# Kernel optimization log

Measured on AMD Instinct MI355X. Metric: run time of the kernel, lower is better.

## Reference

```python
import jax, jax.numpy as jnp
import numpy as np

H, TD, NUM_NODES = 128, 32, 256
B, N, T = 16, 256, 128


def sinusoidal_pe(t, h, dtype=jnp.float32):
    pos = jnp.arange(t, dtype=dtype)[:, None]                      # [T,1]
    div = jnp.exp(jnp.arange(0, h, 2, dtype=dtype) * (-np.log(10000.0) / h))
    pe = jnp.zeros((t, h), dtype=dtype)
    pe = pe.at[:, 0::2].set(jnp.sin(pos * div))
    pe = pe.at[:, 1::2].set(jnp.cos(pos * div))
    return pe                                                      # [T,H]


def setup_inputs() -> dict:
    key = jax.random.key(0)
    ks = jax.random.split(key, 20)
    lin = lambda k, i, o: jax.random.normal(k, (i, o), jnp.float32) / np.sqrt(i)
    return {
        "xf": jax.random.normal(ks[0], (B, N, T, H), jnp.float32),
        "ex": jax.random.normal(ks[1], (B, T, TD), jnp.float32),
        "nf": jax.random.randint(ks[2], (N,), 0, NUM_NODES),
        "mask": jax.random.randint(ks[3], (B, N, T, H), 0, 2).astype(bool),
        "W_in": lin(ks[4], 3 * H, H), "b_in": jnp.zeros((H,), jnp.float32),
        "W_t": lin(ks[5], TD, H), "b_t": jnp.zeros((H,), jnp.float32),
        "E_node": jax.random.normal(ks[6], (NUM_NODES, H), jnp.float32),
        "W_q": lin(ks[7], H, H), "b_q": jnp.zeros((H,), jnp.float32),
        "W_k": lin(ks[8], H, H), "b_k": jnp.zeros((H,), jnp.float32),
        "W_v": lin(ks[9], H, H), "b_v": jnp.zeros((H,), jnp.float32),
        "W_o": lin(ks[10], H, H), "b_o": jnp.zeros((H,), jnp.float32),
    }


def reference(xf, ex, nf, mask, W_in, b_in, W_t, b_t, E_node,
              W_q, b_q, W_k, b_k, W_v, b_v, W_o, b_o):
    b, n, t, h = xf.shape
    # pos-embed + concat(time, node embeds) + linear + GELU (exact erf, like torch F.gelu)
    pe = sinusoidal_pe(t, h, xf.dtype)                              # [T,H]
    time_e = (ex @ W_t + b_t)[:, None, :, :]                        # [B,1,T,H]
    node_e = E_node[nf][None, :, None, :]                           # [1,N,1,H]
    cat = jnp.concatenate([
        xf + pe,
        jnp.broadcast_to(time_e, (b, n, t, h)),
        jnp.broadcast_to(node_e, (b, n, t, h)),
    ], axis=-1)                                                     # [B,N,T,3H]
    x = jax.nn.gelu(cat @ W_in + b_in, approximate=False)           # [B,N,T,H]
    # attention over T per (B,N)
    q = x @ W_q + b_q
    k = x @ W_k + b_k
    v = x @ W_v + b_v
    scores = jnp.einsum('bnsh,bnth->bnst', q, k) * (1.0 / np.sqrt(h))
    A = jnp.nan_to_num(jax.nn.softmax(scores, axis=-1), nan=0.0)    # [B,N,T,T]
    # masked-confidence reduction (detached A in original)
    t_masking = jnp.all(mask, axis=-1)[:, :, None, :].astype(A.dtype)  # [B,N,1,T]
    conf = 1.0 - jnp.sum(jax.lax.stop_gradient(A) * t_masking, axis=-1)  # [B,N,T]
    rec = jnp.einsum('bnst,bnth->bnsh', A, v)                       # [B,N,T,H]
    rec = rec @ W_o + b_o
    return rec, conf
```

## Files before the change

### kernel.cpp

```cpp
#include <hip/hip_runtime.h>
#include <hip/hip_bf16.h>
#include <stdint.h>


typedef __bf16 bf16;
typedef __bf16 bf16x4 __attribute__((ext_vector_type(4)));
typedef __bf16 bf16x8 __attribute__((ext_vector_type(8)));
typedef float  f32x4  __attribute__((ext_vector_type(4)));

#define MFMA16(a, b, c) __builtin_amdgcn_mfma_f32_16x16x32_bf16((a), (b), (c), 0, 0, 0)

__device__ __forceinline__ int allBytesNonzero(unsigned v) {
    return ((v - 0x01010101u) & ~v & 0x80808080u) == 0u;
}

__device__ __forceinline__ bf16x8 cvt8(const float* p) {
    float4 f0 = *reinterpret_cast<const float4*>(p);
    float4 f1 = *reinterpret_cast<const float4*>(p + 4);
    bf16x8 r;
    r[0] = (bf16)f0.x; r[1] = (bf16)f0.y; r[2] = (bf16)f0.z; r[3] = (bf16)f0.w;
    r[4] = (bf16)f1.x; r[5] = (bf16)f1.y; r[6] = (bf16)f1.z; r[7] = (bf16)f1.w;
    return r;
}

__device__ __forceinline__ float gelu_erf(float v) {
    float x  = v * 0.70710678118654752f;
    float ax = fabsf(x);
    float t  = __builtin_amdgcn_rcpf(1.0f + 0.3275911f * ax);
    float p  = ((((1.061405429f * t - 1.453152027f) * t + 1.421413741f) * t
                 - 0.284496736f) * t + 0.254829592f) * t;
    float er = 1.0f - p * __expf(-ax * ax);
    er = copysignf(er, x);
    return 0.5f * v * (1.0f + er);
}

__global__ void prep_weights(const float* __restrict__ W_in, bf16* __restrict__ dst)
{
    int idx = blockIdx.x * 256 + threadIdx.x;
    int h = idx >> 7, k = idx & 127;
    dst[h * 128 + k] = (bf16)W_in[k * 128 + h];
}

__global__ void prep_G(const float* __restrict__ Wq, const float* __restrict__ Wk,
                       const float* __restrict__ bq, bf16* __restrict__ mstore,
                       float* __restrict__ vvec)
{
    const int a = blockIdx.x, bb = threadIdx.x;
    __shared__ float wqa[128];
    wqa[bb] = Wq[a * 128 + bb];
    __syncthreads();
    float acc = 0.f;
    for (int k = 0; k < 128; ++k) acc += wqa[k] * Wk[bb * 128 + k];
    mstore[a * 128 + bb] = (bf16)acc;
    if (a == 0) {
        float av = 0.f;
        for (int j = 0; j < 128; ++j) av += Wk[bb * 128 + j] * bq[j];
        vvec[bb] = av;
    }
}

__global__ void prep_N(const float* __restrict__ Wv, const float* __restrict__ Wo,
                       const float* __restrict__ bv, const float* __restrict__ bo,
                       bf16* __restrict__ nstore, float* __restrict__ bias2)
{
    const int h = blockIdx.x, h2 = threadIdx.x;
    __shared__ float wvh[128];
    wvh[h2] = Wv[h * 128 + h2];
    __syncthreads();
    float acc = 0.f;
    for (int j = 0; j < 128; ++j) acc += wvh[j] * Wo[j * 128 + h2];
    nstore[h2 * 128 + h] = (bf16)acc;
    if (h == 0) {
        float b2 = 0.f;
        for (int j = 0; j < 128; ++j) b2 += bv[j] * Wo[j * 128 + h2];
        bias2[h2] = b2 + bo[h2];
    }
}

__global__ void prep_npart(const int* __restrict__ nf, const float* __restrict__ E_node,
                           const float* __restrict__ W_in, float* __restrict__ npart)
{
    int n = blockIdx.x, h = threadIdx.x;
    int node = nf[n];
    const float* e = E_node + node * 128;
    float acc = 0.f;
    for (int k = 0; k < 128; ++k) acc += e[k] * W_in[(256 + k) * 128 + h];
    npart[n * 128 + h] = acc;
}

__global__ void prep_bias(const float* __restrict__ ex, const float* __restrict__ W_t,
                          const float* __restrict__ b_t, const float* __restrict__ W_in,
                          const float* __restrict__ b_in, float* __restrict__ biasT)
{
    const int bt = blockIdx.x;
    const int t = bt & 127;
    const int h = threadIdx.x;
    __shared__ float te[128];
    float v = b_t[h];
    const float* exr = ex + (size_t)bt * 32;
    for (int d = 0; d < 32; ++d) v += exr[d] * W_t[d * 128 + h];
    te[h] = v;
    __syncthreads();
    float acc = b_in[h];
    const float ninv = -9.210340371976184f / 128.0f;
    for (int j = 0; j < 64; ++j) {
        float div = expf((float)(2 * j) * ninv);
        float ang = (float)t * div;
        acc += sinf(ang) * W_in[(2 * j) * 128 + h] + cosf(ang) * W_in[(2 * j + 1) * 128 + h];
    }
    for (int k = 0; k < 128; ++k) acc += te[k] * W_in[(128 + k) * 128 + h];
    biasT[(size_t)bt * 128 + h] = acc;
}

#define STAGE_ISSUE(SRC)                                                        \
    {                                                                           \
        _Pragma("unroll")                                                       \
        for (int i = 0; i < 4; ++i)                                             \
            stg[i] = *reinterpret_cast<const bf16x8*>((SRC) + (tid + i * 512) * 8); \
    }
#define STAGE_WRITE()                                                           \
    {                                                                           \
        _Pragma("unroll")                                                       \
        for (int i = 0; i < 4; ++i) {                                           \
            int m_ = tid + i * 512;                                             \
            int row_ = m_ >> 4, slot_ = m_ & 15;                                \
            *reinterpret_cast<bf16x8*>(&sW[row_ * 128 + 8 * (slot_ ^ (row_ & 15))]) = stg[i]; \
        }                                                                       \
    }

__global__ __launch_bounds__(512, 4) void fused_main(
    const float* __restrict__ xf, const unsigned char* __restrict__ mask,
    const bf16* __restrict__ wsW, const float* __restrict__ biasT,
    const float* __restrict__ npart, const float* __restrict__ vvec,
    const float* __restrict__ bias2, float* __restrict__ out)
{
    const bf16* W1T = wsW;
    const bf16* Mst = wsW + 16384;
    const bf16* Nst = wsW + 32768;

    __shared__ bf16 sW[16384];
    __shared__ bf16 sKV[128][136];
    __shared__ bf16 sT[8][16][40];
    __shared__ __align__(16) float sTm[128];
    __shared__ __align__(16) float sWt[128];

    const int bn = blockIdx.x;
    const int b  = bn >> 8;
    const int n  = bn & 255;
    const int tid  = (int)threadIdx.x;
    const int w    = tid >> 6;
    const int lane = tid & 63;
    const int c = lane & 15;
    const int g = lane >> 4;
    const int s0 = w << 4;

    const f32x4 FZ = {0.f, 0.f, 0.f, 0.f};
    bf16x8 stg[4];
    bf16* patch = &sT[w][0][0];

    if (tid < 128) {
        const uint4* mp = reinterpret_cast<const uint4*>(mask + ((size_t)bn * 128 + tid) * 128);
        int ok = 1;
        #pragma unroll
        for (int i = 0; i < 8; ++i) {
            uint4 u = mp[i];
            ok &= allBytesNonzero(u.x) & allBytesNonzero(u.y)
                & allBytesNonzero(u.z) & allBytesNonzero(u.w);
        }
        sTm[tid] = ok ? 1.0f : 0.0f;
    }

    STAGE_ISSUE(W1T);
    bf16x8 af[4];
    {
        const float* xfb = xf + (size_t)bn * 16384;
        #pragma unroll
        for (int kk = 0; kk < 4; ++kk)
            af[kk] = cvt8(xfb + (s0 + c) * 128 + kk * 32 + g * 8);
    }
    STAGE_WRITE();
    __syncthreads();

    STAGE_ISSUE(Mst);
    bf16x8 xb[4];
    {
        f32x4 acc[8];
        #pragma unroll
        for (int ht = 0; ht < 8; ++ht) acc[ht] = FZ;
        #pragma unroll
        for (int kk = 0; kk < 4; ++kk) {
            const int k0 = kk * 32 + g * 8;
            #pragma unroll
            for (int ht = 0; ht < 8; ++ht) {
                bf16x8 aw = *reinterpret_cast<const bf16x8*>(
                    &sW[(ht * 16 + c) * 128 + (k0 ^ ((c & 15) << 3))]);
                acc[ht] = MFMA16(aw, af[kk], acc[ht]);
            }
        }
        const float* biasB = biasT + (size_t)b * 16384;
        const float* npRow = npart + n * 128;
        const int t = s0 + c;
        bf16x4 pk[8];
        #pragma unroll
        for (int ht = 0; ht < 8; ++ht) {
            const int hb = ht * 16 + g * 4;
            const float4 bb  = *reinterpret_cast<const float4*>(biasB + t * 128 + hb);
            const float4 np4 = *reinterpret_cast<const float4*>(npRow + hb);
            const float bbr[4] = {bb.x + np4.x, bb.y + np4.y, bb.z + np4.z, bb.w + np4.w};
            #pragma unroll
            for (int r = 0; r < 4; ++r)
                pk[ht][r] = (bf16)gelu_erf(acc[ht][r] + bbr[r]);
        }
        #pragma unroll
        for (int kk = 0; kk < 4; ++kk) {
            *reinterpret_cast<bf16x4*>(patch + c * 40 + g * 4)      = pk[2 * kk];
            *reinterpret_cast<bf16x4*>(patch + c * 40 + 16 + g * 4) = pk[2 * kk + 1];
            xb[kk] = *reinterpret_cast<const bf16x8*>(patch + c * 40 + g * 8);
        }
    }
    __syncthreads();

    STAGE_WRITE();
    __syncthreads();

    STAGE_ISSUE(Nst);
    {
        f32x4 acc[8];
        #pragma unroll
        for (int ht = 0; ht < 8; ++ht) acc[ht] = FZ;
        #pragma unroll
        for (int kk = 0; kk < 4; ++kk) {
            const int k0 = kk * 32 + g * 8;
            #pragma unroll
            for (int ht = 0; ht < 8; ++ht) {
                bf16x8 aw = *reinterpret_cast<const bf16x8*>(
                    &sW[(ht * 16 + c) * 128 + (k0 ^ ((c & 15) << 3))]);
                acc[ht] = MFMA16(aw, xb[kk], acc[ht]);
            }
        }
        const int t = s0 + c;
        #pragma unroll
        for (int ht = 0; ht < 8; ++ht) {
            bf16x4 pk;
            #pragma unroll
            for (int r = 0; r < 4; ++r) pk[r] = (bf16)acc[ht][r];
            *reinterpret_cast<bf16x4*>(&sKV[t][ht * 16 + g * 4]) = pk;
        }
        float wd = 0.f;
        #pragma unroll
        for (int kk = 0; kk < 4; ++kk) {
            const float4 vA = *reinterpret_cast<const float4*>(vvec + kk * 32 + g * 8);
            const float4 vB = *reinterpret_cast<const float4*>(vvec + kk * 32 + g * 8 + 4);
            wd += (float)xb[kk][0] * vA.x + (float)xb[kk][1] * vA.y
                + (float)xb[kk][2] * vA.z + (float)xb[kk][3] * vA.w
                + (float)xb[kk][4] * vB.x + (float)xb[kk][5] * vB.y
                + (float)xb[kk][6] * vB.z + (float)xb[kk][7] * vB.w;
        }
        wd += __shfl_xor(wd, 16);
        wd += __shfl_xor(wd, 32);
        if (g == 0) sWt[t] = wd;
    }
    __syncthreads();

    STAGE_WRITE();
    __syncthreads();

    const float rs = 0.08838834764831845f;
    float l0 = 1.f;
    bf16x8 xp[4];

    {
        f32x4 sc[8];
        #pragma unroll
        for (int rt = 0; rt < 8; ++rt) sc[rt] = FZ;
        #pragma unroll
        for (int kk = 0; kk < 4; ++kk) {
            const int k0 = kk * 32 + g * 8;
            #pragma unroll
            for (int rt = 0; rt < 8; ++rt) {
                bf16x8 ay = *reinterpret_cast<const bf16x8*>(&sKV[rt * 16 + c][k0]);
                sc[rt] = MFMA16(ay, xb[kk], sc[rt]);
            }
        }
        #pragma unroll
        for (int rt = 0; rt < 8; ++rt) {
            const float4 wt4 = *reinterpret_cast<const float4*>(&sWt[rt * 16 + g * 4]);
            sc[rt][0] += wt4.x; sc[rt][1] += wt4.y;
            sc[rt][2] += wt4.z; sc[rt][3] += wt4.w;
        }
        float m = -3.0e38f;
        #pragma unroll
        for (int rt = 0; rt < 8; ++rt)
            #pragma unroll
            for (int r = 0; r < 4; ++r) m = fmaxf(m, sc[rt][r]);
        m = fmaxf(m, __shfl_xor(m, 16));
        m = fmaxf(m, __shfl_xor(m, 32));
        float ls = 0.f, wsum = 0.f;
        #pragma unroll
        for (int rt = 0; rt < 8; ++rt) {
            const float4 tm4 = *reinterpret_cast<const float4*>(&sTm[rt * 16 + g * 4]);
            const float tmr[4] = {tm4.x, tm4.y, tm4.z, tm4.w};
            #pragma unroll
            for (int r = 0; r < 4; ++r) {
                float p = __expf((sc[rt][r] - m) * rs);
                sc[rt][r] = p;
                ls += p;
                wsum += p * tmr[r];
            }
        }
        ls   += __shfl_xor(ls, 16);   ls   += __shfl_xor(ls, 32);
        wsum += __shfl_xor(wsum, 16); wsum += __shfl_xor(wsum, 32);
        l0 = ls;
        if (g == 0)
            out[(size_t)67108864 + (size_t)bn * 128 + s0 + c] = 1.0f - wsum / ls;
        bf16x4 pkP[8];
        #pragma unroll
        for (int rt = 0; rt < 8; ++rt)
            #pragma unroll
            for (int r = 0; r < 4; ++r) pkP[rt][r] = (bf16)sc[rt][r];
        #pragma unroll
        for (int kk = 0; kk < 4; ++kk) {
            *reinterpret_cast<bf16x4*>(patch + c * 40 + g * 4)      = pkP[2 * kk];
            *reinterpret_cast<bf16x4*>(patch + c * 40 + 16 + g * 4) = pkP[2 * kk + 1];
            xp[kk] = *reinterpret_cast<const bf16x8*>(patch + c * 40 + g * 8);
        }
    }

    bf16x4 vpk[8];
    {
        f32x4 acc[8];
        #pragma unroll
        for (int ct = 0; ct < 8; ++ct) acc[ct] = FZ;
        #pragma unroll
        for (int kk = 0; kk < 4; ++kk) {
            const int k0 = kk * 32 + g * 8;
            #pragma unroll
            for (int ct = 0; ct < 8; ++ct) {
                bf16x8 bw = *reinterpret_cast<const bf16x8*>(
                    &sW[(ct * 16 + c) * 128 + (k0 ^ ((c & 15) << 3))]);
                acc[ct] = MFMA16(xb[kk], bw, acc[ct]);
            }
        }
        #pragma unroll
        for (int ct = 0; ct < 8; ++ct)
            #pragma unroll
            for (int r = 0; r < 4; ++r)
                vpk[ct][r] = (bf16)acc[ct][r];
    }
    __syncthreads();

    {
        #pragma unroll
        for (int ct = 0; ct < 8; ++ct)
            *reinterpret_cast<bf16x4*>(&sKV[ct * 16 + c][s0 + g * 4]) = vpk[ct];
    }
    __syncthreads();

    {
        f32x4 rc[8];
        #pragma unroll
        for (int rt = 0; rt < 8; ++rt) rc[rt] = FZ;
        #pragma unroll
        for (int kk = 0; kk < 4; ++kk) {
            const int k0 = kk * 32 + g * 8;
            #pragma unroll
            for (int rt = 0; rt < 8; ++rt) {
                bf16x8 avf = *reinterpret_cast<const bf16x8*>(&sKV[rt * 16 + c][k0]);
                rc[rt] = MFMA16(avf, xp[kk], rc[rt]);
            }
        }
        const float inv0 = __builtin_amdgcn_rcpf(l0);
        float* outb = out + (size_t)bn * 16384 + (size_t)(s0 + c) * 128;
        #pragma unroll
        for (int rt = 0; rt < 8; ++rt) {
            const int hb = rt * 16 + g * 4;
            const float4 b2 = *reinterpret_cast<const float4*>(bias2 + hb);
            float4 v;
            v.x = rc[rt][0] * inv0 + b2.x;
            v.y = rc[rt][1] * inv0 + b2.y;
            v.z = rc[rt][2] * inv0 + b2.z;
            v.w = rc[rt][3] * inv0 + b2.w;
            *reinterpret_cast<float4*>(outb + hb) = v;
        }
    }
}

extern "C" void kernel_launch(void* const* d_in, const int* in_sizes, int n_in,
                              void* d_out, int out_size, void* d_ws, size_t ws_size,
                              hipStream_t stream)
{
    (void)in_sizes; (void)n_in; (void)out_size; (void)ws_size;
    const float* xf     = (const float*)d_in[0];
    const float* ex     = (const float*)d_in[1];
    const int*   nf     = (const int*)d_in[2];
    const unsigned char* mask = (const unsigned char*)d_in[3];
    const float* W_in   = (const float*)d_in[4];
    const float* b_in   = (const float*)d_in[5];
    const float* W_t    = (const float*)d_in[6];
    const float* b_t    = (const float*)d_in[7];
    const float* E_node = (const float*)d_in[8];
    const float* W_q    = (const float*)d_in[9];
    const float* b_q    = (const float*)d_in[10];
    const float* W_k    = (const float*)d_in[11];
    const float* b_k    = (const float*)d_in[12];
    const float* W_v    = (const float*)d_in[13];
    const float* b_v    = (const float*)d_in[14];
    const float* W_o    = (const float*)d_in[15];
    const float* b_o    = (const float*)d_in[16];
    (void)b_k;
    float* out = (float*)d_out;

    bf16*  wsW    = (bf16*)d_ws;
    bf16*  mstore = wsW + 16384;
    bf16*  nstore = wsW + 32768;
    float* biasT  = (float*)((char*)d_ws + 98304);
    float* npart  = (float*)((char*)d_ws + 1146880);
    float* vvec   = (float*)((char*)d_ws + 1277952);
    float* bias2  = (float*)((char*)d_ws + 1278464);

    prep_weights<<<64, 256, 0, stream>>>(W_in, wsW);
    prep_G<<<128, 128, 0, stream>>>(W_q, W_k, b_q, mstore, vvec);
    prep_N<<<128, 128, 0, stream>>>(W_v, W_o, b_v, b_o, nstore, bias2);
    prep_npart<<<256, 128, 0, stream>>>(nf, E_node, W_in, npart);
    prep_bias<<<2048, 128, 0, stream>>>(ex, W_t, b_t, W_in, b_in, biasT);
    fused_main<<<4096, 512, 0, stream>>>(xf, mask, wsW, biasT, npart,
                                         vvec, bias2, out);
}
```

Before: 255.0 us.

## Merge prep kernels, precompute PE sin/cos, raise MFMA priority, move V projection earlier

Four small weight-prep kernels become one launch that picks its job from the block index, which cuts launch overhead. prep_bias now computes the sinusoidal sin/cos values once per block into shared memory instead of once per thread. In the main kernel, MFMA loops are wrapped in s_setprio to favour matrix issue, and the V projection runs before the softmax so it can overlap the exp work. The softmax exponent also becomes a single fma. These changes raise register pressure in the fused section because vpk is held live longer.

```diff
diff --git a/kernel.cpp b/kernel.cpp
--- a/kernel.cpp
+++ b/kernel.cpp
@@ -34,58 +34,52 @@
     return 0.5f * v * (1.0f + er);
 }
 
-__global__ void prep_weights(const float* __restrict__ W_in, bf16* __restrict__ dst)
+__global__ void prep_all(const float* __restrict__ W_in, const float* __restrict__ Wq,
+                         const float* __restrict__ Wk, const float* __restrict__ bq,
+                         const float* __restrict__ Wv, const float* __restrict__ Wo,
+                         const float* __restrict__ bv, const float* __restrict__ bo,
+                         const int* __restrict__ nf, const float* __restrict__ E_node,
+                         bf16* __restrict__ wsW, bf16* __restrict__ mstore,
+                         bf16* __restrict__ nstore, float* __restrict__ vvec,
+                         float* __restrict__ bias2, float* __restrict__ npart)
 {
-    int idx = blockIdx.x * 256 + threadIdx.x;
-    int h = idx >> 7, k = idx & 127;
-    dst[h * 128 + k] = (bf16)W_in[k * 128 + h];
-}
-
-__global__ void prep_G(const float* __restrict__ Wq, const float* __restrict__ Wk,
-                       const float* __restrict__ bq, bf16* __restrict__ mstore,
-                       float* __restrict__ vvec)
-{
-    const int a = blockIdx.x, bb = threadIdx.x;
-    __shared__ float wqa[128];
-    wqa[bb] = Wq[a * 128 + bb];
-    __syncthreads();
-    float acc = 0.f;
-    for (int k = 0; k < 128; ++k) acc += wqa[k] * Wk[bb * 128 + k];
-    mstore[a * 128 + bb] = (bf16)acc;
-    if (a == 0) {
-        float av = 0.f;
-        for (int j = 0; j < 128; ++j) av += Wk[bb * 128 + j] * bq[j];
-        vvec[bb] = av;
-    }
-}
-
-__global__ void prep_N(const float* __restrict__ Wv, const float* __restrict__ Wo,
-                       const float* __restrict__ bv, const float* __restrict__ bo,
-                       bf16* __restrict__ nstore, float* __restrict__ bias2)
-{
-    const int h = blockIdx.x, h2 = threadIdx.x;
-    __shared__ float wvh[128];
-    wvh[h2] = Wv[h * 128 + h2];
-    __syncthreads();
-    float acc = 0.f;
-    for (int j = 0; j < 128; ++j) acc += wvh[j] * Wo[j * 128 + h2];
-    nstore[h2 * 128 + h] = (bf16)acc;
-    if (h == 0) {
-        float b2 = 0.f;
-        for (int j = 0; j < 128; ++j) b2 += bv[j] * Wo[j * 128 + h2];
-        bias2[h2] = b2 + bo[h2];
-    }
-}
-
-__global__ void prep_npart(const int* __restrict__ nf, const float* __restrict__ E_node,
-                           const float* __restrict__ W_in, float* __restrict__ npart)
-{
-    int n = blockIdx.x, h = threadIdx.x;
-    int node = nf[n];
-    const float* e = E_node + node * 128;
-    float acc = 0.f;
-    for (int k = 0; k < 128; ++k) acc += e[k] * W_in[(256 + k) * 128 + h];
-    npart[n * 128 + h] = acc;
+    const int blk = blockIdx.x, t = threadIdx.x;
+    if (blk < 128) {
+        wsW[blk * 128 + t] = (bf16)W_in[t * 128 + blk];
+    } else if (blk < 256) {
+        const int a = blk - 128;
+        __shared__ float wqa[128];
+        wqa[t] = Wq[a * 128 + t];
+        __syncthreads();
+        float acc = 0.f;
+        for (int k = 0; k < 128; ++k) acc += wqa[k] * Wk[t * 128 + k];
+        mstore[a * 128 + t] = (bf16)acc;
+        if (a == 0) {
+            float av = 0.f;
+            for (int j = 0; j < 128; ++j) av += Wk[t * 128 + j] * bq[j];
+            vvec[t] = av;
+        }
+    } else if (blk < 384) {
+        const int h = blk - 256;
+        __shared__ float wvh[128];
+        wvh[t] = Wv[h * 128 + t];
+        __syncthreads();
+        float acc = 0.f;
+        for (int j = 0; j < 128; ++j) acc += wvh[j] * Wo[j * 128 + t];
+        nstore[t * 128 + h] = (bf16)acc;
+        if (h == 0) {
+            float b2 = 0.f;
+            for (int j = 0; j < 128; ++j) b2 += bv[j] * Wo[j * 128 + t];
+            bias2[t] = b2 + bo[t];
+        }
+    } else {
+        const int n = blk - 384;
+        int node = nf[n];
+        const float* e = E_node + node * 128;
+        float acc = 0.f;
+        for (int k = 0; k < 128; ++k) acc += e[k] * W_in[(256 + k) * 128 + t];
+        npart[n * 128 + t] = acc;
+    }
 }
 
 __global__ void prep_bias(const float* __restrict__ ex, const float* __restrict__ W_t,
@@ -96,18 +90,22 @@
     const int t = bt & 127;
     const int h = threadIdx.x;
     __shared__ float te[128];
+    __shared__ float sn[64], cs[64];
     float v = b_t[h];
     const float* exr = ex + (size_t)bt * 32;
     for (int d = 0; d < 32; ++d) v += exr[d] * W_t[d * 128 + h];
     te[h] = v;
+    if (h < 64) {
+        const float ninv = -9.210340371976184f / 128.0f;
+        float div = expf((float)(2 * h) * ninv);
+        float ang = (float)t * div;
+        sn[h] = sinf(ang);
+        cs[h] = cosf(ang);
+    }
     __syncthreads();
     float acc = b_in[h];
-    const float ninv = -9.210340371976184f / 128.0f;
-    for (int j = 0; j < 64; ++j) {
-        float div = expf((float)(2 * j) * ninv);
-        float ang = (float)t * div;
-        acc += sinf(ang) * W_in[(2 * j) * 128 + h] + cosf(ang) * W_in[(2 * j + 1) * 128 + h];
-    }
+    for (int j = 0; j < 64; ++j)
+        acc += sn[j] * W_in[(2 * j) * 128 + h] + cs[j] * W_in[(2 * j + 1) * 128 + h];
     for (int k = 0; k < 128; ++k) acc += te[k] * W_in[(128 + k) * 128 + h];
     biasT[(size_t)bt * 128 + h] = acc;
 }
@@ -187,6 +185,7 @@
         f32x4 acc[8];
         #pragma unroll
         for (int ht = 0; ht < 8; ++ht) acc[ht] = FZ;
+        __builtin_amdgcn_s_setprio(1);
         #pragma unroll
         for (int kk = 0; kk < 4; ++kk) {
             const int k0 = kk * 32 + g * 8;
@@ -197,6 +196,7 @@
                 acc[ht] = MFMA16(aw, af[kk], acc[ht]);
             }
         }
+        __builtin_amdgcn_s_setprio(0);
         const float* biasB = biasT + (size_t)b * 16384;
         const float* npRow = npart + n * 128;
         const int t = s0 + c;
@@ -228,6 +228,7 @@
         f32x4 acc[8];
         #pragma unroll
         for (int ht = 0; ht < 8; ++ht) acc[ht] = FZ;
+        __builtin_amdgcn_s_setprio(1);
         #pragma unroll
         for (int kk = 0; kk < 4; ++kk) {
             const int k0 = kk * 32 + g * 8;
@@ -238,6 +239,7 @@
                 acc[ht] = MFMA16(aw, xb[kk], acc[ht]);
             }
         }
+        __builtin_amdgcn_s_setprio(0);
         const int t = s0 + c;
         #pragma unroll
         for (int ht = 0; ht < 8; ++ht) {
@@ -268,11 +270,13 @@
     const float rs = 0.08838834764831845f;
     float l0 = 1.f;
     bf16x8 xp[4];
+    bf16x4 vpk[8];
 
     {
         f32x4 sc[8];
         #pragma unroll
         for (int rt = 0; rt < 8; ++rt) sc[rt] = FZ;
+        __builtin_amdgcn_s_setprio(1);
         #pragma unroll
         for (int kk = 0; kk < 4; ++kk) {
             const int k0 = kk * 32 + g * 8;
@@ -282,6 +286,31 @@
                 sc[rt] = MFMA16(ay, xb[kk], sc[rt]);
             }
         }
+        __builtin_amdgcn_s_setprio(0);
+
+        {
+            f32x4 acc[8];
+            #pragma unroll
+            for (int ct = 0; ct < 8; ++ct) acc[ct] = FZ;
+            __builtin_amdgcn_s_setprio(1);
+            #pragma unroll
+            for (int kk = 0; kk < 4; ++kk) {
+                const int k0 = kk * 32 + g * 8;
+                #pragma unroll
+                for (int ct = 0; ct < 8; ++ct) {
+                    bf16x8 bw = *reinterpret_cast<const bf16x8*>(
+                        &sW[(ct * 16 + c) * 128 + (k0 ^ ((c & 15) << 3))]);
+                    acc[ct] = MFMA16(xb[kk], bw, acc[ct]);
+                }
+            }
+            __builtin_amdgcn_s_setprio(0);
+            #pragma unroll
+            for (int ct = 0; ct < 8; ++ct)
+                #pragma unroll
+                for (int r = 0; r < 4; ++r)
+                    vpk[ct][r] = (bf16)acc[ct][r];
+        }
+
         #pragma unroll
         for (int rt = 0; rt < 8; ++rt) {
             const float4 wt4 = *reinterpret_cast<const float4*>(&sWt[rt * 16 + g * 4]);
@@ -295,6 +324,7 @@
             for (int r = 0; r < 4; ++r) m = fmaxf(m, sc[rt][r]);
         m = fmaxf(m, __shfl_xor(m, 16));
         m = fmaxf(m, __shfl_xor(m, 32));
+        const float mrs = m * rs;
         float ls = 0.f, wsum = 0.f;
         #pragma unroll
         for (int rt = 0; rt < 8; ++rt) {
@@ -302,7 +332,7 @@
             const float tmr[4] = {tm4.x, tm4.y, tm4.z, tm4.w};
             #pragma unroll
             for (int r = 0; r < 4; ++r) {
-                float p = __expf((sc[rt][r] - m) * rs);
+                float p = __expf(__builtin_fmaf(sc[rt][r], rs, -mrs));
                 sc[rt][r] = p;
                 ls += p;
                 wsum += p * tmr[r];
@@ -325,28 +355,6 @@
             xp[kk] = *reinterpret_cast<const bf16x8*>(patch + c * 40 + g * 8);
         }
     }
-
-    bf16x4 vpk[8];
-    {
-        f32x4 acc[8];
-        #pragma unroll
-        for (int ct = 0; ct < 8; ++ct) acc[ct] = FZ;
-        #pragma unroll
-        for (int kk = 0; kk < 4; ++kk) {
-            const int k0 = kk * 32 + g * 8;
-            #pragma unroll
-            for (int ct = 0; ct < 8; ++ct) {
-                bf16x8 bw = *reinterpret_cast<const bf16x8*>(
-                    &sW[(ct * 16 + c) * 128 + (k0 ^ ((c & 15) << 3))]);
-                acc[ct] = MFMA16(xb[kk], bw, acc[ct]);
-            }
-        }
-        #pragma unroll
-        for (int ct = 0; ct < 8; ++ct)
-            #pragma unroll
-            for (int r = 0; r < 4; ++r)
-                vpk[ct][r] = (bf16)acc[ct][r];
-    }
     __syncthreads();
 
     {
@@ -360,6 +368,7 @@
         f32x4 rc[8];
         #pragma unroll
         for (int rt = 0; rt < 8; ++rt) rc[rt] = FZ;
+        __builtin_amdgcn_s_setprio(1);
         #pragma unroll
         for (int kk = 0; kk < 4; ++kk) {
             const int k0 = kk * 32 + g * 8;
@@ -369,6 +378,7 @@
                 rc[rt] = MFMA16(avf, xp[kk], rc[rt]);
             }
         }
+        __builtin_amdgcn_s_setprio(0);
         const float inv0 = __builtin_amdgcn_rcpf(l0);
         float* outb = out + (size_t)bn * 16384 + (size_t)(s0 + c) * 128;
         #pragma unroll
@@ -418,10 +428,9 @@
     float* vvec   = (float*)((char*)d_ws + 1277952);
     float* bias2  = (float*)((char*)d_ws + 1278464);
 
-    prep_weights<<<64, 256, 0, stream>>>(W_in, wsW);
-    prep_G<<<128, 128, 0, stream>>>(W_q, W_k, b_q, mstore, vvec);
-    prep_N<<<128, 128, 0, stream>>>(W_v, W_o, b_v, b_o, nstore, bias2);
-    prep_npart<<<256, 128, 0, stream>>>(nf, E_node, W_in, npart);
+    prep_all<<<640, 128, 0, stream>>>(W_in, W_q, W_k, b_q, W_v, W_o, b_v, b_o,
+                                      nf, E_node, wsW, mstore, nstore,
+                                      vvec, bias2, npart);
     prep_bias<<<2048, 128, 0, stream>>>(ex, W_t, b_t, W_in, b_in, biasT);
     fused_main<<<4096, 512, 0, stream>>>(xf, mask, wsW, biasT, npart,
                                          vvec, bias2, out);
```

Result: faster. 228.9 us (-10.2%).
